# Optimization experiments

Hardware: AMD Instinct MI355X
Metric: run time of the kernel (lower is better)

The kernel has to match this reference:

```python
import jax, jax.numpy as jnp
import numpy as np

N, C, H, W = 4, 256, 128, 128
BLOCK = 8
FWB = H // BLOCK  # feature_size_with_block = 16
N_BBOX = 100
M = N_BBOX * N * FWB * FWB  # 102400 rois


def setup_inputs() -> dict:
    key = jax.random.key(0)
    ks = jax.random.split(key, 6)
    s = 1.0 / np.sqrt(C).astype(np.float32)
    return {
        "feature": jax.random.normal(ks[0], (N, C, H, W), jnp.float32),
        "rois_feature": jax.random.normal(ks[1], (M, C, 1, 1), jnp.float32),
        "W_weight": jax.random.normal(ks[2], (C, C), jnp.float32) * s,
        "b_weight": jnp.zeros((C,), jnp.float32),
        "W_fuse": jax.random.normal(ks[3], (C, C), jnp.float32) * s,
        "b_fuse": jnp.zeros((C,), jnp.float32),
        "W_pw": jax.random.normal(ks[4], (BLOCK * BLOCK, C), jnp.float32) * s,
        "b_pw": jnp.zeros((BLOCK * BLOCK,), jnp.float32),
        "feature_size_with_block": FWB,
    }


def reference(feature, rois_feature, W_weight, b_weight, W_fuse, b_fuse, W_pw, b_pw, feature_size_with_block):
    n, c, h, w = feature.shape
    f = feature_size_with_block
    blk = h // f  # block_size
    m = rois_feature.shape[0]
    n_bbox = m // (n * f * f)

    x = rois_feature[:, :, 0, 0]  # [M, C] (1x1 conv on 1x1 spatial == dense layer)
    feat_w = jax.nn.relu(x @ W_weight.T + b_weight)  # [M, C]
    feat_f = jax.nn.relu(x @ W_fuse.T + b_fuse)      # [M, C]
    point_weight = feat_w @ W_pw.T + b_pw            # [M, B*B]

    # [n_bbox, N, F, F, B, B] -> [N, n_bbox, F, F, B, B]
    pw = point_weight.reshape(n_bbox, n, f, f, blk, blk).transpose(1, 0, 2, 3, 4, 5)
    # feature -> blocks: [N, C, F, B, F, B] -> [N, C, F, F, B, B]
    fb = feature.reshape(n, c, f, blk, f, blk).transpose(0, 1, 2, 4, 3, 5)
    # weighted block-sum without materializing the n_bbox-repeated tensor.
    # torch: sum over (B,B) -> [N,nb,C,F,F], then permute(1,0,3,4,2) -> [nb,N,F,F,C]
    out = jnp.einsum('ncpqab,nkpqab->knpqc', fb, pw)  # [nb, N, F, F, C]
    out = out.reshape(m, c)[:, :, None, None]          # [M, C, 1, 1]
    fused = feat_f[:, :, None, None] + out
    return fused, out
```

## Files before the change

### kernel.cpp

```cpp
#include <hip/hip_runtime.h>

#define NN 4
#define CC 256
#define HH 128
#define FWBv 16
#define BLK 8
#define NBBOX 100
#define MM (NBBOX * NN * FWBv * FWBv)

typedef __attribute__((ext_vector_type(8))) short bf16x8;
typedef __attribute__((ext_vector_type(4))) float f32x4;

__device__ __forceinline__ unsigned short f2bf(float x) {
  union { float f; unsigned int u; } v; v.f = x;
  unsigned int r = v.u + 0x7FFFu + ((v.u >> 16) & 1u);
  return (unsigned short)(r >> 16);
}

__device__ __forceinline__ float bfbits2f(unsigned int hi16) {
  union { float f; unsigned int u; } v; v.u = hi16;
  return v.f;
}

__device__ __forceinline__ unsigned int pk(float a, float b) {
  return (unsigned int)f2bf(a) | ((unsigned int)f2bf(b) << 16);
}

__global__ __launch_bounds__(256) void k_convert(
    const float* __restrict__ Wf, const float* __restrict__ Ww,
    const float* __restrict__ Wpw,
    unsigned short* __restrict__ oWf, unsigned short* __restrict__ oWw,
    unsigned short* __restrict__ oWpw) {
  const int i = blockIdx.x * 256 + threadIdx.x;
  if (i < 8192) {
    const int lane = i & 63, g = (i >> 6) & 15, kc = i >> 10;
    const int row = g * 16 + (lane & 15);
    const int col0 = kc * 32 + (lane >> 4) * 8;
    {
      const float* s = Wf + (size_t)row * 256 + col0;
      const float4 a = *(const float4*)s, b = *(const float4*)(s + 4);
      *(uint4*)(oWf + (size_t)i * 8) =
          make_uint4(pk(a.x, a.y), pk(a.z, a.w), pk(b.x, b.y), pk(b.z, b.w));
    }
    {
      const float* s = Ww + (size_t)row * 256 + col0;
      const float4 a = *(const float4*)s, b = *(const float4*)(s + 4);
      *(uint4*)(oWw + (size_t)i * 8) =
          make_uint4(pk(a.x, a.y), pk(a.z, a.w), pk(b.x, b.y), pk(b.z, b.w));
    }
  } else {
    const int j = i - 8192;
    const int lane = j & 63, g = (j >> 6) & 3, kc = j >> 8;
    const int row = g * 16 + (lane & 15);
    const int col0 = kc * 32 + (lane >> 4) * 8;
    const float* s = Wpw + (size_t)row * 256 + col0;
    const float4 a = *(const float4*)s, b = *(const float4*)(s + 4);
    *(uint4*)(oWpw + (size_t)j * 8) =
        make_uint4(pk(a.x, a.y), pk(a.z, a.w), pk(b.x, b.y), pk(b.z, b.w));
  }
}

__device__ __forceinline__ bf16x8 ld_frag(const unsigned short* __restrict__ W,
                                          int frag, int lane) {
  return *(const bf16x8*)(W + (((size_t)frag * 64 + lane) << 3));
}

__device__ __forceinline__ void bodyR(const bf16x8 aw[4],
                                      const unsigned short (*xsp)[264],
                                      int kcol, int lr, f32x4 acc[4][4]) {
  bf16x8 bx[4];
#pragma unroll
  for (int mt = 0; mt < 4; ++mt)
    bx[mt] = *(const bf16x8*)&xsp[mt * 16 + lr][kcol];
  __builtin_amdgcn_s_setprio(1);
#pragma unroll
  for (int mt = 0; mt < 4; ++mt)
#pragma unroll
    for (int nt = 0; nt < 4; ++nt)
      acc[mt][nt] = __builtin_amdgcn_mfma_f32_16x16x32_bf16(
          aw[nt], bx[mt], acc[mt][nt], 0, 0, 0);
  __builtin_amdgcn_s_setprio(0);
}

__global__ __launch_bounds__(256, 3) void k1(
    const float* __restrict__ rois,
    const unsigned short* __restrict__ Wf,
    const unsigned short* __restrict__ Ww,
    const unsigned short* __restrict__ Wpw,
    const float* __restrict__ bf_, const float* __restrict__ bw_,
    const float* __restrict__ bpw_,
    float* __restrict__ out_slot)
{
  __shared__ __align__(16) unsigned short xs[64][264];
  unsigned short* os = (unsigned short*)out_slot;
  const int t = threadIdx.x;
  const int lane = t & 63, w = t >> 6;
  const int lr = lane & 15, quad = lane >> 4;
  const int row_base = blockIdx.x * 64;
  const int w4 = w * 4;

  bf16x8 aw[2][4];
#pragma unroll
  for (int nt = 0; nt < 4; ++nt) aw[0][nt] = ld_frag(Wf, w4 + nt, lane);

#pragma unroll
  for (int i = 0; i < 16; ++i) {
    const int elem = (i * 256 + t) * 4;
    const int r = elem >> 8, c = elem & 255;
    const float4 v = *(const float4*)(rois + (size_t)row_base * 256 + elem);
    *(uint2*)&xs[r][c] = make_uint2(pk(v.x, v.y), pk(v.z, v.w));
  }
  asm volatile("s_waitcnt lgkmcnt(0)" ::: "memory");
  __builtin_amdgcn_s_barrier();

  f32x4 acc[4][4];
#pragma unroll
  for (int mt = 0; mt < 4; ++mt)
#pragma unroll
    for (int nt = 0; nt < 4; ++nt) acc[mt][nt] = (f32x4){0.f, 0.f, 0.f, 0.f};

#pragma unroll
  for (int kc = 0; kc < 8; ++kc) {
    const unsigned short* nsrc = (kc < 7) ? Wf : Ww;
    const int nkc = (kc < 7) ? kc + 1 : 0;
#pragma unroll
    for (int nt = 0; nt < 4; ++nt)
      aw[(kc + 1) & 1][nt] = ld_frag(nsrc, nkc * 16 + w4 + nt, lane);
    bodyR(aw[kc & 1], xs, kc * 32 + quad * 8, lr, acc);
  }

#pragma unroll
  for (int nt = 0; nt < 4; ++nt) {
    const int col0 = w * 64 + nt * 16 + quad * 4;
    const float4 b4 = *(const float4*)(bf_ + col0);
#pragma unroll
    for (int mt = 0; mt < 4; ++mt) {
      float v0 = acc[mt][nt][0] + b4.x; v0 = v0 > 0.f ? v0 : 0.f;
      float v1 = acc[mt][nt][1] + b4.y; v1 = v1 > 0.f ? v1 : 0.f;
      float v2 = acc[mt][nt][2] + b4.z; v2 = v2 > 0.f ? v2 : 0.f;
      float v3 = acc[mt][nt][3] + b4.w; v3 = v3 > 0.f ? v3 : 0.f;
      *(uint2*)&os[(size_t)(row_base + mt * 16 + lr) * 512 + 128 + col0] =
          make_uint2(pk(v0, v1), pk(v2, v3));
      acc[mt][nt] = (f32x4){0.f, 0.f, 0.f, 0.f};
    }
  }

#pragma unroll
  for (int kc = 0; kc < 8; ++kc) {
    if (kc < 7) {
#pragma unroll
      for (int nt = 0; nt < 4; ++nt)
        aw[(kc + 1) & 1][nt] = ld_frag(Ww, (kc + 1) * 16 + w4 + nt, lane);
    }
    bodyR(aw[kc & 1], xs, kc * 32 + quad * 8, lr, acc);
  }

  bf16x8 apw[8];
#pragma unroll
  for (int idx = 0; idx < 8; ++idx)
    apw[idx] = ld_frag(Wpw, idx * 4 + w, lane);

  __builtin_amdgcn_s_barrier();

#pragma unroll
  for (int nt = 0; nt < 4; ++nt) {
    const int col0 = w * 64 + nt * 16 + quad * 4;
    const float4 b4 = *(const float4*)(bw_ + col0);
#pragma unroll
    for (int mt = 0; mt < 4; ++mt) {
      float v0 = acc[mt][nt][0] + b4.x; v0 = v0 > 0.f ? v0 : 0.f;
      float v1 = acc[mt][nt][1] + b4.y; v1 = v1 > 0.f ? v1 : 0.f;
      float v2 = acc[mt][nt][2] + b4.z; v2 = v2 > 0.f ? v2 : 0.f;
      float v3 = acc[mt][nt][3] + b4.w; v3 = v3 > 0.f ? v3 : 0.f;
      *(uint2*)&xs[mt * 16 + lr][col0] = make_uint2(pk(v0, v1), pk(v2, v3));
    }
  }
  asm volatile("s_waitcnt lgkmcnt(0)" ::: "memory");
  __builtin_amdgcn_s_barrier();

  f32x4 acc2[4];
#pragma unroll
  for (int mt = 0; mt < 4; ++mt) acc2[mt] = (f32x4){0.f, 0.f, 0.f, 0.f};
#pragma unroll
  for (int idx = 0; idx < 8; ++idx) {
    const int kcol = idx * 32 + quad * 8;
    __builtin_amdgcn_s_setprio(1);
#pragma unroll
    for (int mt = 0; mt < 4; ++mt) {
      const bf16x8 bx = *(const bf16x8*)&xs[mt * 16 + lr][kcol];
      acc2[mt] =
          __builtin_amdgcn_mfma_f32_16x16x32_bf16(apw[idx], bx, acc2[mt], 0, 0, 0);
    }
    __builtin_amdgcn_s_setprio(0);
  }
  {
    const int j0 = w * 16 + quad * 4;
    const float4 bj = *(const float4*)(bpw_ + j0);
#pragma unroll
    for (int mt = 0; mt < 4; ++mt) {
      const float v0 = acc2[mt][0] + bj.x, v1 = acc2[mt][1] + bj.y;
      const float v2 = acc2[mt][2] + bj.z, v3 = acc2[mt][3] + bj.w;
      *(uint2*)&os[(size_t)(row_base + mt * 16 + lr) * 512 + j0] =
          make_uint2(pk(v0, v1), pk(v2, v3));
    }
  }
}

__global__ __launch_bounds__(512, 4) void k2(
    const float* __restrict__ feature,
    float* __restrict__ fused_slot,
    float* __restrict__ out_slot)
{
  __shared__ unsigned short fbuf[256][72];
  __shared__ unsigned short pwb[112][72];
  const int t = threadIdx.x;
  const int lane = t & 63, w = t >> 6;
  const int lr = lane & 15, quad = lane >> 4;
  const int d = blockIdx.x;
  const int bid = ((d & 7) << 7) | (d >> 3);
  const int n = bid >> 8, p = (bid >> 4) & 15, q = bid & 15;
  const unsigned short* os = (const unsigned short*)out_slot;

  if (t < 432) {
    const int r = 100 + t / 36, cw = t % 36;
    *(unsigned int*)&pwb[r][cw * 2] = 0u;
  }

  for (int pi = t; pi < 2048; pi += 512) {
    const int c = pi >> 3, a = pi & 7;
    const float* fp =
        feature + (((size_t)n * 256 + c) * 128 + p * 8 + a) * 128 + q * 8;
    const float4 v0 = *(const float4*)fp;
    const float4 v1 = *(const float4*)(fp + 4);
    *(uint4*)&fbuf[c][a * 8] =
        make_uint4(pk(v0.x, v0.y), pk(v0.z, v0.w), pk(v1.x, v1.y), pk(v1.z, v1.w));
  }

  for (int pi = t; pi < 1600; pi += 512) {
    const int k = pi >> 4, ch = pi & 15;
    const uint2 v = *(const uint2*)&os[(size_t)(bid + k * 1024) * 512 + ch * 4];
    *(uint2*)&pwb[k][ch * 4] = v;
  }
  __syncthreads();

  f32x4 acc[7][2];
#pragma unroll
  for (int kt = 0; kt < 7; ++kt)
#pragma unroll
    for (int ct = 0; ct < 2; ++ct) acc[kt][ct] = (f32x4){0.f, 0.f, 0.f, 0.f};
#pragma unroll
  for (int kj = 0; kj < 2; ++kj) {
    const int kk = kj * 32 + quad * 8;
    bf16x8 fa[2];
#pragma unroll
    for (int ct = 0; ct < 2; ++ct)
      fa[ct] = *(const bf16x8*)&fbuf[w * 32 + ct * 16 + lr][kk];
    {
      bf16x8 pa[4];
#pragma unroll
      for (int kt = 0; kt < 4; ++kt)
        pa[kt] = *(const bf16x8*)&pwb[kt * 16 + lr][kk];
      __builtin_amdgcn_s_setprio(1);
#pragma unroll
      for (int kt = 0; kt < 4; ++kt)
#pragma unroll
        for (int ct = 0; ct < 2; ++ct)
          acc[kt][ct] = __builtin_amdgcn_mfma_f32_16x16x32_bf16(
              fa[ct], pa[kt], acc[kt][ct], 0, 0, 0);
      __builtin_amdgcn_s_setprio(0);
    }
    {
      bf16x8 pa[3];
#pragma unroll
      for (int kt = 0; kt < 3; ++kt)
        pa[kt] = *(const bf16x8*)&pwb[(kt + 4) * 16 + lr][kk];
      __builtin_amdgcn_s_setprio(1);
#pragma unroll
      for (int kt = 0; kt < 3; ++kt)
#pragma unroll
        for (int ct = 0; ct < 2; ++ct)
          acc[kt + 4][ct] = __builtin_amdgcn_mfma_f32_16x16x32_bf16(
              fa[ct], pa[kt], acc[kt + 4][ct], 0, 0, 0);
      __builtin_amdgcn_s_setprio(0);
    }
  }

  uint2 ffp[7][2];
#pragma unroll
  for (int kt = 0; kt < 7; ++kt) {
    const int k = kt * 16 + lr;
    if (k < 100) {
      const size_t ro = (size_t)(bid + k * 1024) * 512;
#pragma unroll
      for (int ct = 0; ct < 2; ++ct) {
        const int c0 = w * 32 + ct * 16 + quad * 4;
        ffp[kt][ct] = *(const uint2*)&os[ro + 128 + c0];
      }
    }
  }

  asm volatile("s_waitcnt vmcnt(0)" ::: "memory");
  __builtin_amdgcn_s_barrier();

#pragma unroll
  for (int kt = 0; kt < 7; ++kt) {
    const int k = kt * 16 + lr;
    if (k < 100) {
      const size_t ro = (size_t)(bid + k * 1024) * 256;
#pragma unroll
      for (int ct = 0; ct < 2; ++ct) {
        const int c0 = w * 32 + ct * 16 + quad * 4;
        float4 v;
        v.x = acc[kt][ct][0];
        v.y = acc[kt][ct][1];
        v.z = acc[kt][ct][2];
        v.w = acc[kt][ct][3];
        *(float4*)(out_slot + ro + c0) = v;
        const uint2 ff = ffp[kt][ct];
        float4 f;
        f.x = v.x + bfbits2f(ff.x << 16);
        f.y = v.y + bfbits2f(ff.x & 0xffff0000u);
        f.z = v.z + bfbits2f(ff.y << 16);
        f.w = v.w + bfbits2f(ff.y & 0xffff0000u);
        *(float4*)(fused_slot + ro + c0) = f;
      }
    }
  }
}

extern "C" void kernel_launch(void* const* d_in, const int* in_sizes, int n_in,
                              void* d_out, int out_size, void* d_ws, size_t ws_size,
                              hipStream_t stream) {
  const float* feature = (const float*)d_in[0];
  const float* rois = (const float*)d_in[1];
  const float* Ww = (const float*)d_in[2];
  const float* bw = (const float*)d_in[3];
  const float* Wf = (const float*)d_in[4];
  const float* bfv = (const float*)d_in[5];
  const float* Wpw = (const float*)d_in[6];
  const float* bpw = (const float*)d_in[7];

  unsigned short* wsWf = (unsigned short*)d_ws;
  unsigned short* wsWw = wsWf + 256 * 256;
  unsigned short* wsWpw = wsWw + 256 * 256;

  float* fused_slot = (float*)d_out;
  float* out_slot = fused_slot + (size_t)MM * 256;

  k_convert<<<40, 256, 0, stream>>>(Wf, Ww, Wpw, wsWf, wsWw, wsWpw);
  k1<<<MM / 64, 256, 0, stream>>>(rois, wsWf, wsWw, wsWpw, bfv, bw, bpw,
                                  out_slot);
  k2<<<NN * FWBv * FWBv, 512, 0, stream>>>(feature, fused_slot, out_slot);
}
```

Baseline: 422.7 us.

## Split k2 across channel halves with duplicated point weights in scratch layout

k2 now runs twice as many 256-thread blocks, each handling half of the 256 channels for one spatial block, which halves its shared memory and register footprint. To support this, k1 writes point weights twice and lays out the fuse activations so each channel half sits next to its own copy of the point weights in the 512-short scratch row. The aim is more parallelism and occupancy in k2 at the cost of an extra duplicated store in k1 and re-reading the point weights in both halves.

Measured after the change: 430.5 us. No clear change (+1.9%).

```diff
diff --git a/kernel.cpp b/kernel.cpp
--- a/kernel.cpp
+++ b/kernel.cpp
@@ -98,6 +98,7 @@
   const int lr = lane & 15, quad = lane >> 4;
   const int row_base = blockIdx.x * 64;
   const int w4 = w * 4;
+  const int zbase = (w < 2) ? 64 : 192;
 
   bf16x8 aw[2][4];
 #pragma unroll
@@ -139,7 +140,7 @@
       float v1 = acc[mt][nt][1] + b4.y; v1 = v1 > 0.f ? v1 : 0.f;
       float v2 = acc[mt][nt][2] + b4.z; v2 = v2 > 0.f ? v2 : 0.f;
       float v3 = acc[mt][nt][3] + b4.w; v3 = v3 > 0.f ? v3 : 0.f;
-      *(uint2*)&os[(size_t)(row_base + mt * 16 + lr) * 512 + 128 + col0] =
+      *(uint2*)&os[(size_t)(row_base + mt * 16 + lr) * 512 + zbase + col0] =
           make_uint2(pk(v0, v1), pk(v2, v3));
       acc[mt][nt] = (f32x4){0.f, 0.f, 0.f, 0.f};
     }
@@ -200,45 +201,51 @@
     for (int mt = 0; mt < 4; ++mt) {
       const float v0 = acc2[mt][0] + bj.x, v1 = acc2[mt][1] + bj.y;
       const float v2 = acc2[mt][2] + bj.z, v3 = acc2[mt][3] + bj.w;
-      *(uint2*)&os[(size_t)(row_base + mt * 16 + lr) * 512 + j0] =
-          make_uint2(pk(v0, v1), pk(v2, v3));
-    }
-  }
-}
-
-__global__ __launch_bounds__(512, 4) void k2(
+      const uint2 pv = make_uint2(pk(v0, v1), pk(v2, v3));
+      const size_t rb = (size_t)(row_base + mt * 16 + lr) * 512;
+      *(uint2*)&os[rb + j0] = pv;
+      *(uint2*)&os[rb + 256 + j0] = pv;
+    }
+  }
+}
+
+__global__ __launch_bounds__(256, 4) void k2(
     const float* __restrict__ feature,
     float* __restrict__ fused_slot,
     float* __restrict__ out_slot)
 {
-  __shared__ unsigned short fbuf[256][72];
+  __shared__ unsigned short fbuf[128][72];
   __shared__ unsigned short pwb[112][72];
   const int t = threadIdx.x;
   const int lane = t & 63, w = t >> 6;
   const int lr = lane & 15, quad = lane >> 4;
   const int d = blockIdx.x;
-  const int bid = ((d & 7) << 7) | (d >> 3);
+  const int L = ((d & 7) << 8) | (d >> 3);
+  const int bid = L >> 1, half = L & 1;
   const int n = bid >> 8, p = (bid >> 4) & 15, q = bid & 15;
   const unsigned short* os = (const unsigned short*)out_slot;
-
-  if (t < 432) {
-    const int r = 100 + t / 36, cw = t % 36;
+  const int zf = 64 + (half << 8);
+
+  for (int z = t; z < 432; z += 256) {
+    const int r = 100 + z / 36, cw = z % 36;
     *(unsigned int*)&pwb[r][cw * 2] = 0u;
   }
 
-  for (int pi = t; pi < 2048; pi += 512) {
-    const int c = pi >> 3, a = pi & 7;
+  for (int pi = t; pi < 1024; pi += 256) {
+    const int cl = pi >> 3, a = pi & 7;
+    const int c = (half << 7) | cl;
     const float* fp =
         feature + (((size_t)n * 256 + c) * 128 + p * 8 + a) * 128 + q * 8;
     const float4 v0 = *(const float4*)fp;
     const float4 v1 = *(const float4*)(fp + 4);
-    *(uint4*)&fbuf[c][a * 8] =
+    *(uint4*)&fbuf[cl][a * 8] =
         make_uint4(pk(v0.x, v0.y), pk(v0.z, v0.w), pk(v1.x, v1.y), pk(v1.z, v1.w));
   }
 
-  for (int pi = t; pi < 1600; pi += 512) {
+  for (int pi = t; pi < 1600; pi += 256) {
     const int k = pi >> 4, ch = pi & 15;
-    const uint2 v = *(const uint2*)&os[(size_t)(bid + k * 1024) * 512 + ch * 4];
+    const uint2 v = *(const uint2*)&os[(size_t)(bid + k * 1024) * 512 +
+                                      (half << 8) + ch * 4];
     *(uint2*)&pwb[k][ch * 4] = v;
   }
   __syncthreads();
@@ -293,8 +300,8 @@
       const size_t ro = (size_t)(bid + k * 1024) * 512;
 #pragma unroll
       for (int ct = 0; ct < 2; ++ct) {
-        const int c0 = w * 32 + ct * 16 + quad * 4;
-        ffp[kt][ct] = *(const uint2*)&os[ro + 128 + c0];
+        const int c0l = w * 32 + ct * 16 + quad * 4;
+        ffp[kt][ct] = *(const uint2*)&os[ro + zf + c0l];
       }
     }
   }
@@ -306,23 +313,23 @@
   for (int kt = 0; kt < 7; ++kt) {
     const int k = kt * 16 + lr;
     if (k < 100) {
-      const size_t ro = (size_t)(bid + k * 1024) * 256;
+      const size_t ro = (size_t)(bid + k * 1024) * 256 + (half << 7);
 #pragma unroll
       for (int ct = 0; ct < 2; ++ct) {
-        const int c0 = w * 32 + ct * 16 + quad * 4;
+        const int c0l = w * 32 + ct * 16 + quad * 4;
         float4 v;
         v.x = acc[kt][ct][0];
         v.y = acc[kt][ct][1];
         v.z = acc[kt][ct][2];
         v.w = acc[kt][ct][3];
-        *(float4*)(out_slot + ro + c0) = v;
+        *(float4*)(out_slot + ro + c0l) = v;
         const uint2 ff = ffp[kt][ct];
         float4 f;
         f.x = v.x + bfbits2f(ff.x << 16);
         f.y = v.y + bfbits2f(ff.x & 0xffff0000u);
         f.z = v.z + bfbits2f(ff.y << 16);
         f.w = v.w + bfbits2f(ff.y & 0xffff0000u);
-        *(float4*)(fused_slot + ro + c0) = f;
+        *(float4*)(fused_slot + ro + c0l) = f;
       }
     }
   }
@@ -350,5 +357,5 @@
   k_convert<<<40, 256, 0, stream>>>(Wf, Ww, Wpw, wsWf, wsWw, wsWpw);
   k1<<<MM / 64, 256, 0, stream>>>(rois, wsWf, wsWw, wsWpw, bfv, bw, bpw,
                                   out_slot);
-  k2<<<NN * FWBv * FWBv, 512, 0, stream>>>(feature, fused_slot, out_slot);
-}
+  k2<<<2 * NN * FWBv * FWBv, 256, 0, stream>>>(feature, fused_slot, out_slot);
+}
```
